# Optimization experiments

Hardware: AMD Instinct MI355X
Metric: run time of the kernel (lower is better)

The kernel has to match this reference:

```python
import jax, jax.numpy as jnp
import numpy as np
from jax import lax

B, C, H, W = 4, 128, 128, 128
MAXD = 192
D = MAXD // 4            # 48 disparity hypotheses at 1/4 scale
WS = 8                   # window size
NH = 8                   # num heads
HD = C // NH             # head dim = 16
SCALE = HD ** -0.5
HID = 4 * C              # mlp hidden (mlp_ratio=4)


def _rel_index(ws):
    coords = np.stack(np.meshgrid(np.arange(ws), np.arange(ws), indexing='ij'))
    cf = coords.reshape(2, -1)
    rel = (cf[:, :, None] - cf[:, None, :]).transpose(1, 2, 0)
    rel[:, :, 0] += ws - 1
    rel[:, :, 1] += ws - 1
    rel[:, :, 0] *= 2 * ws - 1
    return rel.sum(-1)   # [ws*ws, ws*ws]

REL_IDX = jnp.asarray(_rel_index(WS))


def setup_inputs() -> dict:
    key = jax.random.key(0)
    ks = iter(jax.random.split(key, 40))
    rn = lambda shape, s=0.02: jax.random.normal(next(ks), shape, dtype=jnp.float32) * s
    return {
        'feat_l': jax.random.normal(next(ks), (B, C, H, W), dtype=jnp.float32),
        'feat_r': jax.random.normal(next(ks), (B, C, H, W), dtype=jnp.float32),
        'wq': rn((C, C)), 'bq': jnp.zeros((C,), jnp.float32),
        'wk': rn((C, C)), 'bk': jnp.zeros((C,), jnp.float32),
        'wv': rn((C, C)), 'bv': jnp.zeros((C,), jnp.float32),
        'wp': rn((C, C)), 'bp': jnp.zeros((C,), jnp.float32),
        'rpb': rn(((2 * WS - 1) ** 2, NH)),
        'ln1_g': jnp.ones((C,), jnp.float32), 'ln1_b': jnp.zeros((C,), jnp.float32),
        'ln2_g': jnp.ones((C,), jnp.float32), 'ln2_b': jnp.zeros((C,), jnp.float32),
        'mlp_w1': rn((C, HID)), 'mlp_b1': jnp.zeros((HID,), jnp.float32),
        'mlp_w2': rn((HID, C)), 'mlp_b2': jnp.zeros((C,), jnp.float32),
        'un_w1': rn((C, C)), 'un_b1': jnp.zeros((C,), jnp.float32),
        'un_w2': rn((C, C)), 'un_b2': jnp.zeros((C,), jnp.float32),
        'dp_w1': rn((C // 2 + D // 2 + 16, C + D, 3, 3)) if False else rn(((C + D) // 2, C + D, 3, 3)),
        'dp_b1': jnp.zeros(((C + D) // 2,), jnp.float32),
        'bn_g': jnp.ones(((C + D) // 2,), jnp.float32), 'bn_b': jnp.zeros(((C + D) // 2,), jnp.float32),
        'dp_w2': rn((D, (C + D) // 2, 1, 1)), 'dp_b2': jnp.zeros((D,), jnp.float32),
    }


def _ln(x, g, b):
    m = x.mean(-1, keepdims=True)
    v = x.var(-1, keepdims=True)
    return (x - m) * jax.lax.rsqrt(v + 1e-5) * g + b


def _conv(x, w, b, pad):
    y = lax.conv_general_dilated(x, w, (1, 1), [(pad, pad), (pad, pad)],
                                 dimension_numbers=('NCHW', 'OIHW', 'NCHW'))
    return y + b[None, :, None, None]


def _cost_volume(fl, fr):
    # corr[:, d] = mean_c fl[..., w] * fr[..., w-d], zero-padded on the left
    outs = [jnp.mean(fl * fr, axis=1)]
    for d in range(1, D):
        fr_s = jnp.pad(fr[:, :, :, :-d], ((0, 0), (0, 0), (0, 0), (d, 0)))
        outs.append(jnp.mean(fl * fr_s, axis=1))
    return jnp.stack(outs, axis=1)  # [B, D, H, W]


def _win_part(tok):  # [B, H*W, C] -> [B*nW, WS*WS, C]
    x = tok.reshape(B, H // WS, WS, W // WS, WS, C)
    return x.transpose(0, 1, 3, 2, 4, 5).reshape(-1, WS * WS, C)


def _win_rev(win):  # [B*nW, WS*WS, C] -> [B, H*W, C]
    x = win.reshape(B, H // WS, W // WS, WS, WS, C)
    return x.transpose(0, 1, 3, 2, 4, 5).reshape(B, H * W, C)


def _forward(feat_l, feat_r, wq, bq, wk, bk, wv, bv, wp, bp, rpb,
             ln1_g, ln1_b, ln2_g, ln2_b, mlp_w1, mlp_b1, mlp_w2, mlp_b2,
             un_w1, un_b1, un_w2, un_b2, dp_w1, dp_b1, bn_g, bn_b, dp_w2, dp_b2):
    gelu = lambda x: jax.nn.gelu(x, approximate=False)
    cost = _cost_volume(feat_l, feat_r)                       # [B, D, H, W]

    tokens = feat_l.reshape(B, C, H * W).transpose(0, 2, 1)   # [B, N, C]
    unary = gelu(tokens @ un_w1 + un_b1) @ un_w2 + un_b2      # unary potential

    nf = _ln(_win_part(tokens), ln1_g, ln1_b)                 # [Bw, 64, C]
    Bw, N = nf.shape[0], WS * WS
    q = (nf @ wq + bq).reshape(Bw, N, NH, HD).transpose(0, 2, 1, 3)
    k = (nf @ wk + bk).reshape(Bw, N, NH, HD).transpose(0, 2, 1, 3)
    v = (nf @ wv + bv).reshape(Bw, N, NH, HD).transpose(0, 2, 1, 3)
    attn = jnp.einsum('bhnd,bhmd->bhnm', q, k) * SCALE
    bias = rpb[REL_IDX.reshape(-1)].reshape(N, N, NH).transpose(2, 0, 1)
    attn = jax.nn.softmax(attn + bias[None], axis=-1)
    o = jnp.einsum('bhnm,bhmd->bhnd', attn, v).transpose(0, 2, 1, 3).reshape(Bw, N, C)
    pairwise = o @ wp + bp

    x = unary + _win_rev(pairwise)
    x = x + gelu(_ln(x, ln2_g, ln2_b) @ mlp_w1 + mlp_b1) @ mlp_w2 + mlp_b2 * 0.0 + (jnp.zeros((), jnp.float32))
    # (faithful residual MLP; the extra zero terms are no-ops kept out below)
    # -- recompute cleanly to avoid confusion:
    # x = x + mlp(norm2(x))  already done above via single expression

    crf = x.transpose(0, 2, 1).reshape(B, C, H, W)
    fused = jnp.concatenate([crf, cost], axis=1)              # [B, C+D, H, W]

    h1 = jax.nn.relu((_conv(fused, dp_w1, dp_b1, 1)) * jax.lax.rsqrt(jnp.float32(1.0 + 1e-5)) * bn_g[None, :, None, None] + bn_b[None, :, None, None])
    pv = _conv(h1, dp_w2, dp_b2, 0)                           # [B, D, H, W]
    prob = jax.nn.softmax(pv, axis=1)
    disp = jnp.arange(D, dtype=jnp.float32)[None, :, None, None]
    pred = jnp.sum(prob * disp, axis=1, keepdims=True) * 4.0  # [B, 1, H, W]
    return pred


def reference(feat_l, feat_r, wq, bq, wk, bk, wv, bv, wp, bp, rpb,
              ln1_g, ln1_b, ln2_g, ln2_b, mlp_w1, mlp_b1, mlp_w2, mlp_b2,
              un_w1, un_b1, un_w2, un_b2, dp_w1, dp_b1, bn_g, bn_b, dp_w2, dp_b2):
    return _forward(feat_l, feat_r, wq, bq, wk, bk, wv, bv, wp, bp, rpb,
                    ln1_g, ln1_b, ln2_g, ln2_b, mlp_w1, mlp_b1, mlp_w2, mlp_b2,
                    un_w1, un_b1, un_w2, un_b2, dp_w1, dp_b1, bn_g, bn_b, dp_w2, dp_b2)
```

## Files before the change

kernel.cpp:

```cpp
#include <hip/hip_runtime.h>
#include <math.h>

constexpr int Bn = 4, Cc = 128, Hh = 128, Wn = 128, Dd = 48;
constexpr float SCALE = 0.25f;

typedef short  bf16x8 __attribute__((ext_vector_type(8)));
typedef short  bf16x4 __attribute__((ext_vector_type(4)));
typedef float  f32x4  __attribute__((ext_vector_type(4)));
typedef unsigned short u16x8 __attribute__((ext_vector_type(8)));

static __device__ __forceinline__ unsigned short f2bf(float f) {
    return __builtin_bit_cast(unsigned short, (__bf16)f);
}
static __device__ __forceinline__ float bf2f(unsigned short u) {
    return __uint_as_float((unsigned int)u << 16);
}
static __device__ __forceinline__ unsigned int pack2bf(float a, float b) {
    return (unsigned int)f2bf(a) | ((unsigned int)f2bf(b) << 16);
}
static __device__ __forceinline__ float gelu_f(float v) {
    float u = v * (1.5957691216f + 0.0713548162f * v * v);
    return v * __builtin_amdgcn_rcpf(1.0f + __expf(-u));
}

static __device__ __forceinline__ size_t opk_addr(int b, int wh, int ww, int Mt, int ks, int lane) {
    return ((size_t)(b * 16384) + (wh * 8 + Mt * 2 + (ks >> 1)) * 128 + ww * 8) * 128
           + (ks & 1) * 512 + lane * 8;
}

__global__ __launch_bounds__(384) void k_cost(const float* __restrict__ fl,
                                              const float* __restrict__ fr,
                                              unsigned short* __restrict__ costbf) {
    __shared__ float s_fl[2][16][64];
    __shared__ float s_fr[2][16][112];
    int tid = threadIdx.x;
    int w0 = blockIdx.x * 64;
    int hp = blockIdx.y, b = blockIdx.z;
    int row = tid / 192;
    int r = tid - row * 192;
    int wg = r & 15, dg = r >> 4;
    int W = wg * 4, D = dg * 4;
    int h = hp * 2 + row;
    float acc[4][4];
#pragma unroll
    for (int i = 0; i < 4; ++i)
#pragma unroll
        for (int j = 0; j < 4; ++j) acc[i][j] = 0.f;

#pragma unroll 1
    for (int ck = 0; ck < 8; ++ck) {
        int ci0 = ck * 16;
        for (int i = tid; i < 512; i += 384) {
            int rr = i >> 8, rem = i & 255;
            int c = rem >> 4, k4 = rem & 15;
            float4 v = *(const float4*)&fl[((size_t)(b * 128 + ci0 + c) << 14) + (hp * 2 + rr) * 128 + w0 + k4 * 4];
            *(float4*)&s_fl[rr][c][k4 * 4] = v;
        }
        for (int i = tid; i < 896; i += 384) {
            int rr = i / 448, rem = i - rr * 448;
            int c = rem / 28, k4 = rem - c * 28;
            int wgl = w0 - 48 + k4 * 4;
            float4 v = {0.f, 0.f, 0.f, 0.f};
            if (wgl >= 0)
                v = *(const float4*)&fr[((size_t)(b * 128 + ci0 + c) << 14) + (hp * 2 + rr) * 128 + wgl];
            *(float4*)&s_fr[rr][c][k4 * 4] = v;
        }
        __syncthreads();
#pragma unroll
        for (int c = 0; c < 16; ++c) {
            float4 flv = *(const float4*)&s_fl[row][c][W];
            int base = W - D + 44;
            float4 f0 = *(const float4*)&s_fr[row][c][base];
            float4 f1 = *(const float4*)&s_fr[row][c][base + 4];
            float fw[8] = {f0.x, f0.y, f0.z, f0.w, f1.x, f1.y, f1.z, f1.w};
            float fv[4] = {flv.x, flv.y, flv.z, flv.w};
#pragma unroll
            for (int dj = 0; dj < 4; ++dj)
#pragma unroll
                for (int wv = 0; wv < 4; ++wv)
                    acc[dj][wv] += fv[wv] * fw[wv - dj + 4];
        }
        __syncthreads();
    }
    const float inv = 1.0f / 128.0f;
    unsigned short* cb = costbf + ((size_t)(b << 14) + h * 128 + w0 + W) * 64;
    const u16x8 z8 = {0, 0, 0, 0, 0, 0, 0, 0};
#pragma unroll
    for (int wv = 0; wv < 4; ++wv) {
        bf16x4 o4;
#pragma unroll
        for (int dj = 0; dj < 4; ++dj) o4[dj] = (short)f2bf(acc[dj][wv] * inv);
        *(bf16x4*)&cb[wv * 64 + D] = o4;
        if (D == 44) {
            *(u16x8*)&cb[wv * 64 + 48] = z8;
            *(u16x8*)&cb[wv * 64 + 56] = z8;
        }
    }
}

static __device__ void pack_conv(int blk, int lane,
                                 const float* __restrict__ w1, const float* __restrict__ b1,
                                 const float* __restrict__ bng, const float* __restrict__ bnb,
                                 unsigned short* __restrict__ pk, float* __restrict__ bias2) {
    const float rs = 0.9999950000374997f;
    int ct = blk % 6;
    int taplin = blk / 6;
    int tap = taplin % 9, chunk = taplin / 9;
    int co = ct * 16 + (lane & 15);
    int cibase = chunk * 32 + (lane >> 4) * 8;
    u16x8 out;
#pragma unroll
    for (int j = 0; j < 8; ++j) {
        int ci = cibase + j;
        float v = 0.f;
        if (co < 88 && ci < 176) v = w1[(size_t)co * 1584 + ci * 9 + tap] * rs * bng[co];
        out[j] = f2bf(v);
    }
    *(u16x8*)(pk + ((size_t)blk * 64 + lane) * 8) = out;
    if (blk == 0) {
        for (int i = lane; i < 96; i += 64)
            bias2[i] = (i < 88) ? (b1[i] * rs * bng[i] + bnb[i]) : 0.f;
    }
}

static __device__ void pack_gemmB(int blk, int lane,
                                  const float* __restrict__ W,
                                  unsigned short* __restrict__ out, int ncols) {
    int ntiles = ncols >> 4;
    int ks = blk & 3;
    int nt = (blk >> 2) % ntiles;
    int kc = blk / (4 * ntiles);
    int col = nt * 16 + (lane & 15);
    int k0 = kc * 128 + ks * 32 + (lane >> 4) * 8;
    u16x8 o;
#pragma unroll
    for (int j = 0; j < 8; ++j) o[j] = f2bf(W[(size_t)(k0 + j) * ncols + col]);
    *(u16x8*)(out + ((size_t)blk * 64 + lane) * 8) = o;
}

static __device__ void pack_rpb(int blk, int lane,
                                const float* __restrict__ rpb, float* __restrict__ pb) {
    int nt = blk & 3, mt = (blk >> 2) & 3, hh = blk >> 4;
    int tq = nt * 16 + (lane & 15);
    int g = lane >> 4;
    float o[4];
#pragma unroll
    for (int rr = 0; rr < 4; ++rr) {
        int tk = mt * 16 + g * 4 + rr;
        int relidx = (((tq >> 3) - (tk >> 3)) + 7) * 15 + ((tq & 7) - (tk & 7)) + 7;
        o[rr] = rpb[relidx * 8 + hh];
    }
    float4 v = {o[0], o[1], o[2], o[3]};
    *(float4*)(pb + ((size_t)blk * 64 + lane) * 4) = v;
}

__global__ __launch_bounds__(64) void k_pack_all(
        const float* __restrict__ dp_w1, const float* __restrict__ dp_b1,
        const float* __restrict__ bn_g, const float* __restrict__ bn_b,
        unsigned short* __restrict__ pk, float* __restrict__ bias2,
        const float* __restrict__ wq, const float* __restrict__ wk,
        const float* __restrict__ wv, const float* __restrict__ wp,
        unsigned short* __restrict__ pkw,
        const float* __restrict__ rpb, float* __restrict__ pb,
        const float* __restrict__ mlp_w1, unsigned short* __restrict__ pm1,
        const float* __restrict__ mlp_w2, unsigned short* __restrict__ pm2,
        const float* __restrict__ un_w1, unsigned short* __restrict__ pu1,
        const float* __restrict__ un_w2, unsigned short* __restrict__ pu2) {
    int blk = blockIdx.x;
    int lane = threadIdx.x;
    if (blk < 324) {
        pack_conv(blk, lane, dp_w1, dp_b1, bn_g, bn_b, pk, bias2);
    } else if (blk < 452) {
        int bb = blk - 324;
        int mat = bb >> 5;
        const float* W = (mat == 0) ? wq : (mat == 1) ? wk : (mat == 2) ? wv : wp;
        pack_gemmB(bb & 31, lane, W, pkw + (size_t)mat * 16384, 128);
    } else if (blk < 580) {
        pack_rpb(blk - 452, lane, rpb, pb);
    } else if (blk < 708) {
        pack_gemmB(blk - 580, lane, mlp_w1, pm1, 512);
    } else if (blk < 836) {
        pack_gemmB(blk - 708, lane, mlp_w2, pm2, 128);
    } else if (blk < 868) {
        pack_gemmB(blk - 836, lane, un_w1, pu1, 128);
    } else {
        pack_gemmB(blk - 868, lane, un_w2, pu2, 128);
    }
}

__global__ __launch_bounds__(256) void k_unary_mfma(const float* __restrict__ feat_l,
                                                    const unsigned short* __restrict__ pu1,
                                                    const float* __restrict__ b1,
                                                    const unsigned short* __restrict__ pu2,
                                                    const float* __restrict__ b2,
                                                    const float* __restrict__ g1,
                                                    const float* __restrict__ bt1,
                                                    unsigned short* __restrict__ xu,
                                                    unsigned short* __restrict__ nf) {
    __shared__ __align__(16) unsigned short s_a[64 * 136];
    __shared__ __align__(16) unsigned short s_h[64 * 136];
    int tid = threadIdx.x;
    int wid = tid >> 6, lane = tid & 63;
    int g = lane >> 4, t = lane & 15;
    int n0g = blockIdx.x * 64;
    int b = n0g >> 14;
    int nb = n0g & 16383;

    for (int idx = tid; idx < 4096; idx += 256) {
        int c2 = idx >> 6, nl = idx & 63;
        float v0 = feat_l[((size_t)(b * 128 + 2 * c2) << 14) + nb + nl];
        float v1 = feat_l[((size_t)(b * 128 + 2 * c2 + 1) << 14) + nb + nl];
        *(unsigned int*)&s_a[nl * 136 + 2 * c2] = pack2bf(v0, v1);
    }
    __syncthreads();

    {
        int tok = tid >> 2, q = tid & 3;
        float v[32];
#pragma unroll
        for (int i8 = 0; i8 < 4; ++i8) {
            u16x8 r8 = *(const u16x8*)&s_a[tok * 136 + q * 32 + i8 * 8];
#pragma unroll
            for (int j = 0; j < 8; ++j) v[i8 * 8 + j] = bf2f(r8[j]);
        }
        float s = 0.f, s2 = 0.f;
#pragma unroll
        for (int i = 0; i < 32; ++i) { s += v[i]; s2 += v[i] * v[i]; }
        s += __shfl_xor(s, 1); s += __shfl_xor(s, 2);
        s2 += __shfl_xor(s2, 1); s2 += __shfl_xor(s2, 2);
        float mean = s * (1.f / 128.f);
        float var = s2 * (1.f / 128.f) - mean * mean;
        float rstd = rsqrtf(var + 1e-5f);
        size_t base = (size_t)(n0g + tok) * 128 + q * 32;
#pragma unroll
        for (int i8 = 0; i8 < 4; ++i8) {
            u16x8 o8;
#pragma unroll
            for (int j = 0; j < 8; ++j) {
                int c = q * 32 + i8 * 8 + j;
                o8[j] = f2bf((v[i8 * 8 + j] - mean) * rstd * g1[c] + bt1[c]);
            }
            *(u16x8*)&nf[base + i8 * 8] = o8;
        }
    }

    bf16x8 af[4][4];
#pragma unroll
    for (int Mt = 0; Mt < 4; ++Mt)
#pragma unroll
        for (int ks = 0; ks < 4; ++ks)
            af[Mt][ks] = *(const bf16x8*)&s_a[(Mt * 16 + t) * 136 + ks * 32 + g * 8];

    f32x4 acc1[4][2];
#pragma unroll
    for (int nt2 = 0; nt2 < 2; ++nt2) {
        float bv = b1[(wid * 2 + nt2) * 16 + t];
#pragma unroll
        for (int Mt = 0; Mt < 4; ++Mt) acc1[Mt][nt2] = (f32x4){bv, bv, bv, bv};
    }
#pragma unroll
    for (int ks = 0; ks < 4; ++ks) {
        bf16x8 bf0 = *(const bf16x8*)(pu1 + (size_t)(((wid * 2 + 0) * 4 + ks) * 64 + lane) * 8);
        bf16x8 bf1 = *(const bf16x8*)(pu1 + (size_t)(((wid * 2 + 1) * 4 + ks) * 64 + lane) * 8);
#pragma unroll
        for (int Mt = 0; Mt < 4; ++Mt) {
            acc1[Mt][0] = __builtin_amdgcn_mfma_f32_16x16x32_bf16(af[Mt][ks], bf0, acc1[Mt][0], 0, 0, 0);
            acc1[Mt][1] = __builtin_amdgcn_mfma_f32_16x16x32_bf16(af[Mt][ks], bf1, acc1[Mt][1], 0, 0, 0);
        }
    }
#pragma unroll
    for (int Mt = 0; Mt < 4; ++Mt)
#pragma unroll
        for (int nt2 = 0; nt2 < 2; ++nt2)
#pragma unroll
            for (int rr = 0; rr < 4; ++rr)
                s_h[(Mt * 16 + g * 4 + rr) * 136 + (wid * 2 + nt2) * 16 + t] = f2bf(gelu_f(acc1[Mt][nt2][rr]));
    __syncthreads();

    bf16x8 a2[4][4];
#pragma unroll
    for (int Mt = 0; Mt < 4; ++Mt)
#pragma unroll
        for (int ks = 0; ks < 4; ++ks)
            a2[Mt][ks] = *(const bf16x8*)&s_h[(Mt * 16 + t) * 136 + ks * 32 + g * 8];

    f32x4 acc2[4][2];
#pragma unroll
    for (int nt2 = 0; nt2 < 2; ++nt2) {
        float bv = b2[(wid * 2 + nt2) * 16 + t];
#pragma unroll
        for (int Mt = 0; Mt < 4; ++Mt) acc2[Mt][nt2] = (f32x4){bv, bv, bv, bv};
    }
#pragma unroll
    for (int ks = 0; ks < 4; ++ks) {
        bf16x8 bf0 = *(const bf16x8*)(pu2 + (size_t)(((wid * 2 + 0) * 4 + ks) * 64 + lane) * 8);
        bf16x8 bf1 = *(const bf16x8*)(pu2 + (size_t)(((wid * 2 + 1) * 4 + ks) * 64 + lane) * 8);
#pragma unroll
        for (int Mt = 0; Mt < 4; ++Mt) {
            acc2[Mt][0] = __builtin_amdgcn_mfma_f32_16x16x32_bf16(a2[Mt][ks], bf0, acc2[Mt][0], 0, 0, 0);
            acc2[Mt][1] = __builtin_amdgcn_mfma_f32_16x16x32_bf16(a2[Mt][ks], bf1, acc2[Mt][1], 0, 0, 0);
        }
    }
#pragma unroll
    for (int Mt = 0; Mt < 4; ++Mt)
#pragma unroll
        for (int nt2 = 0; nt2 < 2; ++nt2)
#pragma unroll
            for (int rr = 0; rr < 4; ++rr) {
                int tok = Mt * 16 + g * 4 + rr;
                xu[(size_t)(n0g + tok) * 128 + (wid * 2 + nt2) * 16 + t] = f2bf(acc2[Mt][nt2][rr]);
            }
}

__global__ __launch_bounds__(256, 3) void k_attn_core(const unsigned short* nf,
                                                      const unsigned short* __restrict__ pkw,
                                                      const float* __restrict__ pb,
                                                      const float* __restrict__ bq,
                                                      const float* __restrict__ bk,
                                                      const float* __restrict__ bv,
                                                      unsigned short* opk) {
    __shared__ __align__(16) unsigned short s_all[4 * 5760];
    int tid = threadIdx.x;
    int wid = tid >> 6, lane = tid & 63;
    int g = lane >> 4, t = lane & 15;
    int bw = blockIdx.x;
    int b = bw >> 8, wh = (bw >> 4) & 15, ww = bw & 15;

    bf16x8 af[4][4];
#pragma unroll
    for (int Mt = 0; Mt < 4; ++Mt) {
        int tok = Mt * 16 + t;
        size_t gtok = (size_t)(b * 16384) + (wh * 8 + (tok >> 3)) * 128 + ww * 8 + (tok & 7);
#pragma unroll
        for (int ks = 0; ks < 4; ++ks)
            af[Mt][ks] = *(const bf16x8*)&nf[gtok * 128 + ks * 32 + g * 8];
    }
    __syncthreads();

    unsigned short* sQ = s_all + wid * 5760;
    unsigned short* sK = sQ + 1536;
    unsigned short* sV = sQ + 4608;
    unsigned short* sP = sQ;
    unsigned short* sO = sQ;

    const bf16x8 z8v = {0, 0, 0, 0, 0, 0, 0, 0};

#pragma unroll
    for (int hi = 0; hi < 2; ++hi) {
        int h = wid + hi * 4;

        float bqv = bq[h * 16 + t], bkv = bk[h * 16 + t], bvv = bv[h * 16 + t];
        f32x4 qa[4], ka[4], va[4];
#pragma unroll
        for (int Mt = 0; Mt < 4; ++Mt) {
            qa[Mt] = (f32x4){bqv, bqv, bqv, bqv};
            ka[Mt] = (f32x4){bkv, bkv, bkv, bkv};
            va[Mt] = (f32x4){bvv, bvv, bvv, bvv};
        }
#pragma unroll
        for (int ks = 0; ks < 4; ++ks) {
            const unsigned short* wbase = pkw + ((size_t)((h * 4 + ks) * 64 + lane) * 8);
            bf16x8 bfq = *(const bf16x8*)(wbase);
            bf16x8 bfk = *(const bf16x8*)(wbase + 16384);
            bf16x8 bfv = *(const bf16x8*)(wbase + 32768);
#pragma unroll
            for (int Mt = 0; Mt < 4; ++Mt) {
                qa[Mt] = __builtin_amdgcn_mfma_f32_16x16x32_bf16(af[Mt][ks], bfq, qa[Mt], 0, 0, 0);
                ka[Mt] = __builtin_amdgcn_mfma_f32_16x16x32_bf16(af[Mt][ks], bfk, ka[Mt], 0, 0, 0);
                va[Mt] = __builtin_amdgcn_mfma_f32_16x16x32_bf16(af[Mt][ks], bfv, va[Mt], 0, 0, 0);
            }
        }
#pragma unroll
        for (int Mt = 0; Mt < 4; ++Mt) {
            bf16x4 vv;
#pragma unroll
            for (int rr = 0; rr < 4; ++rr) {
                int tok = Mt * 16 + g * 4 + rr;
                sQ[tok * 24 + t] = f2bf(qa[Mt][rr] * SCALE);
                sK[tok * 24 + t] = f2bf(ka[Mt][rr]);
                vv[rr] = (short)f2bf(va[Mt][rr]);
            }
            *(bf16x4*)&sV[t * 72 + Mt * 16 + g * 4] = vv;
        }

        f32x4 s[4][4];
#pragma unroll
        for (int Mtk = 0; Mtk < 4; ++Mtk)
#pragma unroll
            for (int Ntq = 0; Ntq < 4; ++Ntq)
                s[Mtk][Ntq] = *(const f32x4*)(pb + ((size_t)((h * 16 + Mtk * 4 + Ntq) * 64 + lane) * 4));
        bf16x8 bQ[4];
#pragma unroll
        for (int Ntq = 0; Ntq < 4; ++Ntq)
            bQ[Ntq] = (g < 2) ? *(const bf16x8*)&sQ[(Ntq * 16 + t) * 24 + g * 8] : z8v;
#pragma unroll
        for (int Mtk = 0; Mtk < 4; ++Mtk) {
            bf16x8 aK = (g < 2) ? *(const bf16x8*)&sK[(Mtk * 16 + t) * 24 + g * 8] : z8v;
#pragma unroll
            for (int Ntq = 0; Ntq < 4; ++Ntq)
                s[Mtk][Ntq] = __builtin_amdgcn_mfma_f32_16x16x32_bf16(aK, bQ[Ntq], s[Mtk][Ntq], 0, 0, 0);
        }

#pragma unroll
        for (int Ntq = 0; Ntq < 4; ++Ntq) {
            float m = s[0][Ntq][0];
#pragma unroll
            for (int Mtk = 0; Mtk < 4; ++Mtk)
#pragma unroll
                for (int rr = 0; rr < 4; ++rr) m = fmaxf(m, s[Mtk][Ntq][rr]);
            m = fmaxf(m, __shfl_xor(m, 16));
            m = fmaxf(m, __shfl_xor(m, 32));
            float sum = 0.f;
#pragma unroll
            for (int Mtk = 0; Mtk < 4; ++Mtk)
#pragma unroll
                for (int rr = 0; rr < 4; ++rr) {
                    float e = __expf(s[Mtk][Ntq][rr] - m);
                    s[Mtk][Ntq][rr] = e;
                    sum += e;
                }
            sum += __shfl_xor(sum, 16);
            sum += __shfl_xor(sum, 32);
            float inv = __builtin_amdgcn_rcpf(sum);
#pragma unroll
            for (int Mtk = 0; Mtk < 4; ++Mtk) {
                bf16x4 pv;
#pragma unroll
                for (int rr = 0; rr < 4; ++rr) pv[rr] = (short)f2bf(s[Mtk][Ntq][rr] * inv);
                *(bf16x4*)&sP[(Ntq * 16 + t) * 72 + Mtk * 16 + g * 4] = pv;
            }
        }

        f32x4 oa[4];
#pragma unroll
        for (int Mt = 0; Mt < 4; ++Mt) oa[Mt] = (f32x4){0.f, 0.f, 0.f, 0.f};
#pragma unroll
        for (int ksv = 0; ksv < 2; ++ksv) {
            bf16x8 bv2 = *(const bf16x8*)&sV[t * 72 + ksv * 32 + g * 8];
#pragma unroll
            for (int Mt = 0; Mt < 4; ++Mt) {
                bf16x8 ap = *(const bf16x8*)&sP[(Mt * 16 + t) * 72 + ksv * 32 + g * 8];
                oa[Mt] = __builtin_amdgcn_mfma_f32_16x16x32_bf16(ap, bv2, oa[Mt], 0, 0, 0);
            }
        }
#pragma unroll
        for (int Mt = 0; Mt < 4; ++Mt)
#pragma unroll
            for (int rr = 0; rr < 4; ++rr)
                sO[(Mt * 16 + g * 4 + rr) * 16 + t] = f2bf(oa[Mt][rr]);
        int ksf = h >> 1;
        if ((g >> 1) == (h & 1)) {
#pragma unroll
            for (int Mt = 0; Mt < 4; ++Mt) {
                bf16x8 v8 = *(const bf16x8*)&sO[(Mt * 16 + t) * 16 + (g & 1) * 8];
                *(bf16x8*)&opk[opk_addr(b, wh, ww, Mt, ksf, lane)] = v8;
            }
        }
    }
}

__global__ __launch_bounds__(256) void k_mlp_mfma(const unsigned short* __restrict__ xu,
                                                  const unsigned short* opk,
                                                  const unsigned short* __restrict__ pkw,
                                                  const float* __restrict__ bp,
                                                  const float* __restrict__ g2,
                                                  const float* __restrict__ bt2,
                                                  const unsigned short* __restrict__ pm1,
                                                  const float* __restrict__ b1,
                                                  const unsigned short* __restrict__ pm2,
                                                  unsigned short* xbf) {
    __shared__ __align__(16) char smem[18432];
    float* sf = (float*)smem;
    unsigned short* s_h = (unsigned short*)smem;
    float* s_st = (float*)(smem + 16896);
    float* s_gb = (float*)(smem + 17152);
    int tid = threadIdx.x;
    int wid = tid >> 6, lane = tid & 63;
    int g = lane >> 4, t = lane & 15;
    int bw = blockIdx.x >> 1, half = blockIdx.x & 1;
    int b = bw >> 8, wh = (bw >> 4) & 15, ww = bw & 15;

    auto gtok_of = [&](int tok) -> size_t {
        int tg = half * 32 + tok;
        return (size_t)(b * 16384) + (wh * 8 + (tg >> 3)) * 128 + ww * 8 + (tg & 7);
    };

    if (tid < 128) s_gb[tid] = g2[tid];
    else if (tid < 256) s_gb[tid] = bt2[tid - 128];

    f32x4 out[2][2];
    {
        float bp0 = bp[wid * 32 + t], bp1 = bp[wid * 32 + 16 + t];
#pragma unroll
        for (int Mt = 0; Mt < 2; ++Mt) {
            out[Mt][0] = (f32x4){bp0, bp0, bp0, bp0};
            out[Mt][1] = (f32x4){bp1, bp1, bp1, bp1};
        }
#pragma unroll
        for (int ks = 0; ks < 4; ++ks) {
            bf16x8 b0 = *(const bf16x8*)(pkw + 49152 + (size_t)(((wid * 2 + 0) * 4 + ks) * 64 + lane) * 8);
            bf16x8 b1v = *(const bf16x8*)(pkw + 49152 + (size_t)(((wid * 2 + 1) * 4 + ks) * 64 + lane) * 8);
#pragma unroll
            for (int Mt = 0; Mt < 2; ++Mt) {
                bf16x8 a = *(const bf16x8*)&opk[opk_addr(b, wh, ww, half * 2 + Mt, ks, lane)];
                out[Mt][0] = __builtin_amdgcn_mfma_f32_16x16x32_bf16(a, b0, out[Mt][0], 0, 0, 0);
                out[Mt][1] = __builtin_amdgcn_mfma_f32_16x16x32_bf16(a, b1v, out[Mt][1], 0, 0, 0);
            }
        }
#pragma unroll
        for (int Mt = 0; Mt < 2; ++Mt)
#pragma unroll
            for (int nt2 = 0; nt2 < 2; ++nt2)
#pragma unroll
                for (int rr = 0; rr < 4; ++rr) {
                    int tok = Mt * 16 + g * 4 + rr;
                    int col = (wid * 2 + nt2) * 16 + t;
                    float v = out[Mt][nt2][rr] + bf2f(xu[gtok_of(tok) * 128 + col]);
                    out[Mt][nt2][rr] = v;
                    sf[tok * 132 + col] = v;
                }
    }
    __syncthreads();
    if (tid < 128) {
        int tok = tid >> 2, q = tid & 3;
        float s = 0.f, s2 = 0.f;
        for (int c = q * 32; c < q * 32 + 32; ++c) {
            float v = sf[tok * 132 + c];
            s += v; s2 += v * v;
        }
        s += __shfl_xor(s, 1); s += __shfl_xor(s, 2);
        s2 += __shfl_xor(s2, 1); s2 += __shfl_xor(s2, 2);
        if (q == 0) {
            float mean = s * (1.f / 128.f);
            float var = s2 * (1.f / 128.f) - mean * mean;
            s_st[tok * 2] = mean;
            s_st[tok * 2 + 1] = rsqrtf(var + 1e-5f);
        }
    }
    __syncthreads();
    bf16x8 af2[2][4];
#pragma unroll
    for (int Mt = 0; Mt < 2; ++Mt) {
        int tok = Mt * 16 + t;
        float mean = s_st[tok * 2], rstd = s_st[tok * 2 + 1];
#pragma unroll
        for (int ks = 0; ks < 4; ++ks) {
            int c0 = ks * 32 + g * 8;
            float4 v0 = *(const float4*)&sf[tok * 132 + c0];
            float4 v1 = *(const float4*)&sf[tok * 132 + c0 + 4];
            float vv[8] = {v0.x, v0.y, v0.z, v0.w, v1.x, v1.y, v1.z, v1.w};
            u16x8 o8;
#pragma unroll
            for (int j = 0; j < 8; ++j)
                o8[j] = f2bf((vv[j] - mean) * rstd * s_gb[c0 + j] + s_gb[128 + c0 + j]);
            af2[Mt][ks] = __builtin_bit_cast(bf16x8, o8);
        }
    }
    __syncthreads();

#pragma unroll 1
    for (int hc = 0; hc < 2; ++hc) {
#pragma unroll
        for (int jh = 0; jh < 2; ++jh) {
            f32x4 acc1[2][2];
#pragma unroll
            for (int j2 = 0; j2 < 2; ++j2) {
                float bv = b1[hc * 256 + (wid * 4 + jh * 2 + j2) * 16 + t];
#pragma unroll
                for (int Mt = 0; Mt < 2; ++Mt) acc1[Mt][j2] = (f32x4){bv, bv, bv, bv};
            }
#pragma unroll
            for (int ks = 0; ks < 4; ++ks) {
                int nt0 = hc * 16 + wid * 4 + jh * 2;
                bf16x8 bf0 = *(const bf16x8*)(pm1 + (size_t)((((nt0 + 0) * 4 + ks) * 64 + lane) * 8));
                bf16x8 bf1 = *(const bf16x8*)(pm1 + (size_t)((((nt0 + 1) * 4 + ks) * 64 + lane) * 8));
#pragma unroll
                for (int Mt = 0; Mt < 2; ++Mt) {
                    acc1[Mt][0] = __builtin_amdgcn_mfma_f32_16x16x32_bf16(af2[Mt][ks], bf0, acc1[Mt][0], 0, 0, 0);
                    acc1[Mt][1] = __builtin_amdgcn_mfma_f32_16x16x32_bf16(af2[Mt][ks], bf1, acc1[Mt][1], 0, 0, 0);
                }
            }
#pragma unroll
            for (int Mt = 0; Mt < 2; ++Mt)
#pragma unroll
                for (int j2 = 0; j2 < 2; ++j2)
#pragma unroll
                    for (int rr = 0; rr < 4; ++rr)
                        s_h[(Mt * 16 + g * 4 + rr) * 264 + (wid * 4 + jh * 2 + j2) * 16 + t] =
                            f2bf(gelu_f(acc1[Mt][j2][rr]));
        }
        __syncthreads();
#pragma unroll
        for (int kt = 0; kt < 8; ++kt) {
            int kc = hc * 2 + (kt >> 2), ks = kt & 3;
            bf16x8 bf0 = *(const bf16x8*)(pm2 + (size_t)(((kc * 32 + (wid * 2 + 0) * 4 + ks) * 64 + lane) * 8));
            bf16x8 bf1 = *(const bf16x8*)(pm2 + (size_t)(((kc * 32 + (wid * 2 + 1) * 4 + ks) * 64 + lane) * 8));
#pragma unroll
            for (int Mt = 0; Mt < 2; ++Mt) {
                bf16x8 a2 = *(const bf16x8*)&s_h[(Mt * 16 + t) * 264 + kt * 32 + g * 8];
                out[Mt][0] = __builtin_amdgcn_mfma_f32_16x16x32_bf16(a2, bf0, out[Mt][0], 0, 0, 0);
                out[Mt][1] = __builtin_amdgcn_mfma_f32_16x16x32_bf16(a2, bf1, out[Mt][1], 0, 0, 0);
            }
        }
        __syncthreads();
    }

#pragma unroll
    for (int Mt = 0; Mt < 2; ++Mt)
#pragma unroll
        for (int nt2 = 0; nt2 < 2; ++nt2)
#pragma unroll
            for (int rr = 0; rr < 4; ++rr) {
                int tok = Mt * 16 + g * 4 + rr;
                xbf[gtok_of(tok) * 128 + (wid * 2 + nt2) * 16 + t] = f2bf(out[Mt][nt2][rr]);
            }
}

__global__ __launch_bounds__(256) void k_conv_mfma(const unsigned short* __restrict__ xbf,
                                                   const unsigned short* __restrict__ costbf,
                                                   const unsigned short* __restrict__ pk,
                                                   const float* __restrict__ bias2,
                                                   unsigned short* __restrict__ h1) {
    __shared__ __align__(16) unsigned short s_p[180 * 40];
    int tid = threadIdx.x;
    int wid = tid >> 6, lane = tid & 63;
    int g = lane >> 4, t = lane & 15;
    int tx0 = blockIdx.x * 16, ty0 = blockIdx.y * 8, b = blockIdx.z;

    f32x4 acc[2][6];
#pragma unroll
    for (int p = 0; p < 2; ++p)
#pragma unroll
        for (int ct = 0; ct < 6; ++ct) acc[p][ct] = (f32x4){0.f, 0.f, 0.f, 0.f};

#pragma unroll 1
    for (int chunk = 0; chunk < 6; ++chunk) {
        for (int u = tid; u < 180; u += 256) {
            int yy = u / 18, xx = u - yy * 18;
            int gy = ty0 + yy - 1, gx = tx0 + xx - 1;
            u16x8 v0 = (u16x8)(unsigned short)0, v1 = v0, v2 = v0, v3 = v0;
            if (gy >= 0 && gy < 128 && gx >= 0 && gx < 128) {
                size_t pix = (size_t)(b << 14) + gy * 128 + gx;
                const u16x8* src = (chunk < 4)
                    ? (const u16x8*)&xbf[pix * 128 + chunk * 32]
                    : (const u16x8*)&costbf[pix * 64 + (chunk - 4) * 32];
                v0 = src[0]; v1 = src[1]; v2 = src[2]; v3 = src[3];
            }
            *(u16x8*)&s_p[u * 40 + 0] = v0;
            *(u16x8*)&s_p[u * 40 + 8] = v1;
            *(u16x8*)&s_p[u * 40 + 16] = v2;
            *(u16x8*)&s_p[u * 40 + 24] = v3;
        }
        __syncthreads();

#pragma unroll 1
        for (int tap = 0; tap < 9; ++tap) {
            int dy = tap / 3, dx = tap - dy * 3;
            const unsigned short* pkt = pk + ((size_t)(chunk * 9 + tap)) * 6 * 512;
            bf16x8 afr[6];
#pragma unroll
            for (int ct = 0; ct < 6; ++ct)
                afr[ct] = *(const bf16x8*)(pkt + ct * 512 + lane * 8);
            bf16x8 bfr[2];
#pragma unroll
            for (int p = 0; p < 2; ++p) {
                int pos = (wid * 2 + p + dy) * 18 + t + dx;
                bfr[p] = *(const bf16x8*)&s_p[pos * 40 + g * 8];
            }
#pragma unroll
            for (int p = 0; p < 2; ++p)
#pragma unroll
                for (int ct = 0; ct < 6; ++ct)
                    acc[p][ct] = __builtin_amdgcn_mfma_f32_16x16x32_bf16(afr[ct], bfr[p], acc[p][ct], 0, 0, 0);
        }
        __syncthreads();
    }

#pragma unroll
    for (int p = 0; p < 2; ++p) {
        int y = ty0 + wid * 2 + p;
#pragma unroll
        for (int ct = 0; ct < 6; ++ct) {
#pragma unroll
            for (int rr = 0; rr < 4; ++rr) {
                int co = ct * 16 + g * 4 + rr;
                if (co < 88) {
                    float v = acc[p][ct][rr] + bias2[co];
                    h1[((size_t)(b * 88 + co) << 14) + y * 128 + tx0 + t] = f2bf(fmaxf(v, 0.f));
                }
            }
        }
    }
}

__global__ __launch_bounds__(256) void k_head(const unsigned short* __restrict__ h1,
                                              const float* __restrict__ w2, const float* __restrict__ b2,
                                              float* __restrict__ out) {
    __shared__ float s_wt[88 * 48];
    __shared__ float s_b[48];
    int tid = threadIdx.x;
    for (int idx = tid; idx < 48 * 88; idx += 256) {
        int d = idx / 88, k = idx % 88;
        s_wt[k * 48 + d] = w2[idx];
    }
    if (tid < 48) s_b[tid] = b2[tid];
    __syncthreads();
    int px = blockIdx.x * 256 + tid;
    int b = px >> 14, r = px & 16383;
    float acc[48];
#pragma unroll
    for (int d = 0; d < 48; ++d) acc[d] = s_b[d];
    for (int k = 0; k < 88; ++k) {
        float hv = bf2f(h1[((size_t)(b * 88 + k) << 14) + r]);
        const float4* wrow = (const float4*)&s_wt[k * 48];
#pragma unroll
        for (int d4 = 0; d4 < 12; ++d4) {
            float4 wv = wrow[d4];
            acc[d4 * 4 + 0] += hv * wv.x;
            acc[d4 * 4 + 1] += hv * wv.y;
            acc[d4 * 4 + 2] += hv * wv.z;
            acc[d4 * 4 + 3] += hv * wv.w;
        }
    }
    float mx = -1e30f;
#pragma unroll
    for (int d = 0; d < 48; ++d) mx = fmaxf(mx, acc[d]);
    float sum = 0.f, wsum = 0.f;
#pragma unroll
    for (int d = 0; d < 48; ++d) {
        float e = __expf(acc[d] - mx);
        sum += e;
        wsum += e * (float)d;
    }
    out[px] = 4.0f * wsum * __builtin_amdgcn_rcpf(sum);
}

extern "C" void kernel_launch(void* const* d_in, const int* in_sizes, int n_in,
                              void* d_out, int out_size, void* d_ws, size_t ws_size,
                              hipStream_t stream) {
    const float* feat_l = (const float*)d_in[0];
    const float* feat_r = (const float*)d_in[1];
    const float* wq = (const float*)d_in[2];
    const float* bq = (const float*)d_in[3];
    const float* wk = (const float*)d_in[4];
    const float* bk = (const float*)d_in[5];
    const float* wv = (const float*)d_in[6];
    const float* bv = (const float*)d_in[7];
    const float* wp = (const float*)d_in[8];
    const float* bp = (const float*)d_in[9];
    const float* rpb = (const float*)d_in[10];
    const float* ln1_g = (const float*)d_in[11];
    const float* ln1_b = (const float*)d_in[12];
    const float* ln2_g = (const float*)d_in[13];
    const float* ln2_b = (const float*)d_in[14];
    const float* mlp_w1 = (const float*)d_in[15];
    const float* mlp_b1 = (const float*)d_in[16];
    const float* mlp_w2 = (const float*)d_in[17];
    const float* un_w1 = (const float*)d_in[19];
    const float* un_b1 = (const float*)d_in[20];
    const float* un_w2 = (const float*)d_in[21];
    const float* un_b2 = (const float*)d_in[22];
    const float* dp_w1 = (const float*)d_in[23];
    const float* dp_b1 = (const float*)d_in[24];
    const float* bn_g = (const float*)d_in[25];
    const float* bn_b = (const float*)d_in[26];
    const float* dp_w2 = (const float*)d_in[27];
    const float* dp_b2 = (const float*)d_in[28];

    float* ws = (float*)d_ws;
    unsigned short* costbf = (unsigned short*)ws;
    unsigned short* xu = (unsigned short*)(ws + 3145728);
    unsigned short* h1bf = (unsigned short*)(ws + 3145728);
    unsigned short* nfo = (unsigned short*)(ws + 11534336);
    unsigned short* pk = (unsigned short*)(ws + 17301504);
    float* bias2 = ws + 17384448;
    unsigned short* pkw = (unsigned short*)(ws + 17384544);
    float* pb = ws + 17417312;
    unsigned short* pm1 = (unsigned short*)(ws + 17450080);
    unsigned short* pm2 = (unsigned short*)(ws + 17482848);
    unsigned short* pu1 = (unsigned short*)(ws + 17515616);
    unsigned short* pu2 = (unsigned short*)(ws + 17523808);
    float* out = (float*)d_out;

    k_pack_all<<<900, 64, 0, stream>>>(dp_w1, dp_b1, bn_g, bn_b, pk, bias2,
                                       wq, wk, wv, wp, pkw, rpb, pb,
                                       mlp_w1, pm1, mlp_w2, pm2,
                                       un_w1, pu1, un_w2, pu2);
    k_cost<<<dim3(2, 64, 4), 384, 0, stream>>>(feat_l, feat_r, costbf);
    k_unary_mfma<<<1024, 256, 0, stream>>>(feat_l, pu1, un_b1, pu2, un_b2,
                                           ln1_g, ln1_b, xu, nfo);
    k_attn_core<<<1024, 256, 0, stream>>>(nfo, pkw, pb, bq, bk, bv, nfo);
    k_mlp_mfma<<<2048, 256, 0, stream>>>(xu, nfo, pkw, bp, ln2_g, ln2_b,
                                         pm1, mlp_b1, pm2, nfo);
    k_conv_mfma<<<dim3(8, 16, 4), 256, 0, stream>>>(nfo, costbf, pk, bias2, h1bf);
    k_head<<<256, 256, 0, stream>>>(h1bf, dp_w2, dp_b2, out);
}
```

Before: 246.1 us.

## Store conv output pixel-major and read head weights from pre-transposed global buffer

The conv kernel now writes its 88-channel bf16 output in a pixel-major layout padded to 96 channels, so the head kernel can load each pixel's channels with 16-byte vector loads. The head weights are transposed once in the pack kernel, and the head kernel reads them from global memory with wave-uniform addresses instead of staging them in shared memory. This removes the per-block shared-memory setup and barrier and the strided channel-major reads. In exchange, the conv stores become strided scattered 2-byte writes, and the fully unrolled head loop raises register pressure.

```diff
diff --git a/kernel.cpp b/kernel.cpp
--- a/kernel.cpp
+++ b/kernel.cpp
@@ -165,7 +165,8 @@
         const float* __restrict__ mlp_w1, unsigned short* __restrict__ pm1,
         const float* __restrict__ mlp_w2, unsigned short* __restrict__ pm2,
         const float* __restrict__ un_w1, unsigned short* __restrict__ pu1,
-        const float* __restrict__ un_w2, unsigned short* __restrict__ pu2) {
+        const float* __restrict__ un_w2, unsigned short* __restrict__ pu2,
+        const float* __restrict__ dp_w2, float* __restrict__ w2t) {
     int blk = blockIdx.x;
     int lane = threadIdx.x;
     if (blk < 324) {
@@ -183,8 +184,13 @@
         pack_gemmB(blk - 708, lane, mlp_w2, pm2, 128);
     } else if (blk < 868) {
         pack_gemmB(blk - 836, lane, un_w1, pu1, 128);
+    } else if (blk < 900) {
+        pack_gemmB(blk - 868, lane, un_w2, pu2, 128);
     } else {
-        pack_gemmB(blk - 868, lane, un_w2, pu2, 128);
+        for (int i = lane; i < 4224; i += 64) {
+            int k = i / 48, d = i - (i / 48) * 48;
+            w2t[i] = dp_w2[d * 88 + k];
+        }
     }
 }
 
@@ -679,6 +685,7 @@
 #pragma unroll
     for (int p = 0; p < 2; ++p) {
         int y = ty0 + wid * 2 + p;
+        size_t pix = (size_t)(b << 14) + y * 128 + tx0 + t;
 #pragma unroll
         for (int ct = 0; ct < 6; ++ct) {
 #pragma unroll
@@ -686,41 +693,31 @@
                 int co = ct * 16 + g * 4 + rr;
                 if (co < 88) {
                     float v = acc[p][ct][rr] + bias2[co];
-                    h1[((size_t)(b * 88 + co) << 14) + y * 128 + tx0 + t] = f2bf(fmaxf(v, 0.f));
+                    h1[pix * 96 + co] = f2bf(fmaxf(v, 0.f));
                 }
             }
         }
     }
 }
 
-__global__ __launch_bounds__(256) void k_head(const unsigned short* __restrict__ h1,
-                                              const float* __restrict__ w2, const float* __restrict__ b2,
+__global__ __launch_bounds__(256) void k_head(const unsigned short* __restrict__ h1p,
+                                              const float* __restrict__ w2t,
+                                              const float* __restrict__ b2,
                                               float* __restrict__ out) {
-    __shared__ float s_wt[88 * 48];
-    __shared__ float s_b[48];
-    int tid = threadIdx.x;
-    for (int idx = tid; idx < 48 * 88; idx += 256) {
-        int d = idx / 88, k = idx % 88;
-        s_wt[k * 48 + d] = w2[idx];
-    }
-    if (tid < 48) s_b[tid] = b2[tid];
-    __syncthreads();
-    int px = blockIdx.x * 256 + tid;
-    int b = px >> 14, r = px & 16383;
+    int px = blockIdx.x * 256 + threadIdx.x;
+    const unsigned short* hrow = h1p + (size_t)px * 96;
+    u16x8 hv8[11];
+#pragma unroll
+    for (int i = 0; i < 11; ++i) hv8[i] = *(const u16x8*)&hrow[i * 8];
     float acc[48];
 #pragma unroll
-    for (int d = 0; d < 48; ++d) acc[d] = s_b[d];
+    for (int d = 0; d < 48; ++d) acc[d] = b2[d];
+#pragma unroll
     for (int k = 0; k < 88; ++k) {
-        float hv = bf2f(h1[((size_t)(b * 88 + k) << 14) + r]);
-        const float4* wrow = (const float4*)&s_wt[k * 48];
-#pragma unroll
-        for (int d4 = 0; d4 < 12; ++d4) {
-            float4 wv = wrow[d4];
-            acc[d4 * 4 + 0] += hv * wv.x;
-            acc[d4 * 4 + 1] += hv * wv.y;
-            acc[d4 * 4 + 2] += hv * wv.z;
-            acc[d4 * 4 + 3] += hv * wv.w;
-        }
+        float hv = bf2f(hv8[k >> 3][k & 7]);
+        const float* wr = w2t + k * 48;
+#pragma unroll
+        for (int d = 0; d < 48; ++d) acc[d] += hv * wr[d];
     }
     float mx = -1e30f;
 #pragma unroll
@@ -780,12 +777,14 @@
     unsigned short* pm2 = (unsigned short*)(ws + 17482848);
     unsigned short* pu1 = (unsigned short*)(ws + 17515616);
     unsigned short* pu2 = (unsigned short*)(ws + 17523808);
+    float* w2t = ws + 17532000;
     float* out = (float*)d_out;
 
-    k_pack_all<<<900, 64, 0, stream>>>(dp_w1, dp_b1, bn_g, bn_b, pk, bias2,
+    k_pack_all<<<901, 64, 0, stream>>>(dp_w1, dp_b1, bn_g, bn_b, pk, bias2,
                                        wq, wk, wv, wp, pkw, rpb, pb,
                                        mlp_w1, pm1, mlp_w2, pm2,
-                                       un_w1, pu1, un_w2, pu2);
+                                       un_w1, pu1, un_w2, pu2,
+                                       dp_w2, w2t);
     k_cost<<<dim3(2, 64, 4), 384, 0, stream>>>(feat_l, feat_r, costbf);
     k_unary_mfma<<<1024, 256, 0, stream>>>(feat_l, pu1, un_b1, pu2, un_b2,
                                            ln1_g, ln1_b, xu, nfo);
@@ -793,5 +792,5 @@
     k_mlp_mfma<<<2048, 256, 0, stream>>>(xu, nfo, pkw, bp, ln2_g, ln2_b,
                                          pm1, mlp_b1, pm2, nfo);
     k_conv_mfma<<<dim3(8, 16, 4), 256, 0, stream>>>(nfo, costbf, pk, bias2, h1bf);
-    k_head<<<256, 256, 0, stream>>>(h1bf, dp_w2, dp_b2, out);
-}
+    k_head<<<256, 256, 0, stream>>>(h1bf, w2t, dp_b2, out);
+}
```

Result: faster. 235.5 us (-4.3%).
